# Kernel optimization log

Hardware: AMD Instinct MI355X
Metric: run time of the kernel (lower is better)

Reference implementation:

```python
import jax, jax.numpy as jnp
import numpy as np

DIM = 1024
D_STATE = 16
D_CONV = 4
EXPAND = 2
D_INNER = EXPAND * DIM          # 2048
DT_RANK = (DIM + 15) // 16      # 64 (math.ceil(d_model/16))
BSZ = 2
SEQ = 2048


def setup_inputs() -> dict:
    key = jax.random.key(0)
    ks = jax.random.split(key, 8)
    g = lambda k, shape, scale: (jax.random.normal(k, shape, jnp.float32) * scale)
    return {
        "x": g(ks[0], (BSZ, SEQ, DIM), 1.0),
        # in_proj: Linear(d_model -> 2*d_inner, bias=False)
        "W_in": g(ks[1], (2 * D_INNER, DIM), DIM ** -0.5),
        # depthwise causal conv1d: groups=d_inner, kernel d_conv, bias=True
        "conv_w": g(ks[2], (D_INNER, 1, D_CONV), D_CONV ** -0.5),
        "conv_b": jnp.zeros((D_INNER,), jnp.float32),
        # x_proj: Linear(d_inner -> dt_rank + 2*d_state, bias=False)
        "W_xproj": g(ks[3], (DT_RANK + 2 * D_STATE, D_INNER), D_INNER ** -0.5),
        # dt_proj: Linear(dt_rank -> d_inner, bias=True)
        "W_dt": g(ks[4], (D_INNER, DT_RANK), DT_RANK ** -0.5),
        "b_dt": g(ks[5], (D_INNER,), 0.1),
        # S4D-real init: A = -exp(A_log), A_log = log(1..d_state)
        "A_log": jnp.log(jnp.broadcast_to(
            jnp.arange(1, D_STATE + 1, dtype=jnp.float32), (D_INNER, D_STATE))),
        "D": jnp.ones((D_INNER,), jnp.float32),
        # out_proj: Linear(d_inner -> d_model, bias=False)
        "W_out": g(ks[6], (DIM, D_INNER), D_INNER ** -0.5),
        # wrapper LayerNorm(dim)
        "gamma": jnp.ones((DIM,), jnp.float32),
        "beta": jnp.zeros((DIM,), jnp.float32),
    }


def reference(x, W_in, conv_w, conv_b, W_xproj, W_dt, b_dt,
              A_log, D, W_out, gamma, beta):
    B, L, _ = x.shape
    # ---- input projection, split into conv path and gate ----
    xz = x @ W_in.T                              # (B, L, 2*d_inner)
    xc, z = jnp.split(xz, 2, axis=-1)
    # ---- depthwise causal conv1d + SiLU ----
    xt = jnp.transpose(xc, (0, 2, 1))            # (B, d_inner, L)
    conv = jax.lax.conv_general_dilated(
        xt, conv_w, window_strides=(1,), padding=[(D_CONV - 1, 0)],
        dimension_numbers=("NCH", "OIH", "NCH"), feature_group_count=D_INNER)
    u = jax.nn.silu(jnp.transpose(conv + conv_b[None, :, None], (0, 2, 1)))  # (B,L,d_inner)
    # ---- input-dependent delta, B, C ----
    xdbc = u @ W_xproj.T                          # (B, L, dt_rank + 2*d_state)
    dt = xdbc[..., :DT_RANK]
    Bm = xdbc[..., DT_RANK:DT_RANK + D_STATE]     # (B, L, d_state)
    Cm = xdbc[..., DT_RANK + D_STATE:]            # (B, L, d_state)
    delta = jax.nn.softplus(dt @ W_dt.T + b_dt)   # (B, L, d_inner)
    A = -jnp.exp(A_log)                           # (d_inner, d_state)
    # ---- selective scan: h_t = exp(dt*A) h_{t-1} + dt*B_t*u_t ; y_t = <h_t, C_t> ----
    def step(h, inputs):
        d_t, u_t, B_t, C_t = inputs               # (B,d_inner),(B,d_inner),(B,S),(B,S)
        dA = jnp.exp(d_t[:, :, None] * A)         # (B, d_inner, S)
        h = h * dA + (d_t * u_t)[:, :, None] * B_t[:, None, :]
        y = jnp.einsum("bds,bs->bd", h, C_t)
        return h, y
    tm = lambda a: jnp.transpose(a, (1, 0, 2))    # time-major for scan
    h0 = jnp.zeros((B, D_INNER, D_STATE), x.dtype)
    _, ys = jax.lax.scan(step, h0, (tm(delta), tm(u), tm(Bm), tm(Cm)))
    y = jnp.transpose(ys, (1, 0, 2)) + u * D      # skip term D*u
    y = y * jax.nn.silu(z)                        # gate
    out = y @ W_out.T                             # (B, L, dim)
    # ---- wrapper LayerNorm(dim), eps=1e-5 ----
    mean = out.mean(-1, keepdims=True)
    var = out.var(-1, keepdims=True)
    return (out - mean) * jax.lax.rsqrt(var + 1e-5) * gamma + beta
```

## Files before the change

### kernel.cpp

```cpp
#include <hip/hip_runtime.h>
#include <stdint.h>

typedef unsigned short u16;
typedef __bf16 bf16x8 __attribute__((ext_vector_type(8)));
typedef unsigned short u16x8 __attribute__((ext_vector_type(8)));
typedef unsigned short u16x4 __attribute__((ext_vector_type(4)));
typedef float f32x4 __attribute__((ext_vector_type(4)));

#define BSZ 2
#define SEQ 2048
#define DIM 1024
#define D_INNER 2048
#define DT_RANK 64
#define D_STATE 16
#define XPROJ_N 96
#define NCHUNK 32
#define CHUNK_T 64
#define LOG2E 1.44269504f

#define N_X   4194304
#define N_W   4194304
#define N_WX  196608
#define N_WDT 131072
#define N_WO  2097152
#define N_XD  393216

__device__ __forceinline__ float bf2f(u16 h) {
    return __uint_as_float(((unsigned)h) << 16);
}
__device__ __forceinline__ u16 f2bf(float f) {
    unsigned u = __float_as_uint(f);
    unsigned r = (u + 0x7FFFu + ((u >> 16) & 1u)) >> 16;
    return (u16)r;
}

__device__ __forceinline__ f32x4 mfma16(bf16x8 a, bf16x8 b, f32x4 c) {
    return __builtin_amdgcn_mfma_f32_16x16x32_bf16(a, b, c, 0, 0, 0);
}

__device__ __forceinline__ void gload_lds16(const void* g, void* l) {
    __builtin_amdgcn_global_load_lds(
        (const __attribute__((address_space(1))) unsigned int*)(uintptr_t)g,
        (__attribute__((address_space(3))) unsigned int*)(uintptr_t)l,
        16, 0, 0);
}

__device__ __forceinline__ void split4(const float* __restrict__ in,
                                       u16* __restrict__ hi, u16* __restrict__ lo,
                                       long i)
{
    f32x4 v = *(const f32x4*)(in + i);
    u16x4 h, l;
    #pragma unroll
    for (int j = 0; j < 4; j++) {
        u16 hh = f2bf(v[j]);
        h[j] = hh;
        l[j] = f2bf(v[j] - bf2f(hh));
    }
    *(u16x4*)(hi + i) = h;
    *(u16x4*)(lo + i) = l;
}

__global__ __launch_bounds__(256)
void megasplit4(const float* __restrict__ x,  u16* __restrict__ xh,  u16* __restrict__ xl,
                const float* __restrict__ w,  u16* __restrict__ wh,  u16* __restrict__ wl,
                const float* __restrict__ wx, u16* __restrict__ wxh, u16* __restrict__ wxl,
                const float* __restrict__ wd, u16* __restrict__ wdh, u16* __restrict__ wdl)
{
    long i = ((long)blockIdx.x * 256 + threadIdx.x) * 4;
    if (i < N_X) { split4(x, xh, xl, i); return; }
    i -= N_X;
    if (i < N_W) { split4(w, wh, wl, i); return; }
    i -= N_W;
    if (i < N_WX) { split4(wx, wxh, wxl, i); return; }
    i -= N_WX;
    if (i < N_WDT) { split4(wd, wdh, wdl, i); }
}

__global__ __launch_bounds__(512, 2)
void gemm256_xz(const u16* __restrict__ xh, const u16* __restrict__ xl,
                const u16* __restrict__ wh, const u16* __restrict__ wl,
                u16* __restrict__ xc, float* __restrict__ z)
{
    __shared__ u16 lds[49152];

    const int tid  = threadIdx.x;
    const int w    = tid >> 6;
    const int lane = tid & 63;
    const int r16  = lane & 15;
    const int quad = lane >> 4;
    const int wr   = w >> 2;
    const int wc   = w & 3;
    const long m0  = (long)blockIdx.y * 256;
    const long n0  = (long)blockIdx.x * 256;

    const int c0 = tid, c1 = tid + 512;
    const int ma0 = c0 >> 2, kc0 = ((c0 & 3) ^ ((ma0 >> 1) & 3)) * 8;
    const int ma1 = c1 >> 2, kc1 = ((c1 & 3) ^ ((ma1 >> 1) & 3)) * 8;
    const int arow0 = ((int)m0 + ma0) * DIM + kc0;
    const int arow1 = ((int)m0 + ma1) * DIM + kc1;
    const int brow0 = ((int)n0 + ma0) * DIM + kc0;
    const int brow1 = ((int)n0 + ma1) * DIM + kc1;

    int caof[8], cbof[4];
    #pragma unroll
    for (int i = 0; i < 8; i++) {
        int m = wr * 128 + i * 16 + r16;
        caof[i] = (m * 4 + (quad ^ ((m >> 1) & 3))) * 8;
    }
    #pragma unroll
    for (int j = 0; j < 4; j++) {
        int n = wc * 64 + j * 16 + r16;
        cbof[j] = (n * 4 + (quad ^ ((n >> 1) & 3))) * 8;
    }

    f32x4 acc[8][4];
    #pragma unroll
    for (int i = 0; i < 8; i++)
        #pragma unroll
        for (int j = 0; j < 4; j++) acc[i][j] = {0.f, 0.f, 0.f, 0.f};

    gload_lds16(xh + arow0,      lds + c0 * 8);
    gload_lds16(xh + arow1,      lds + c1 * 8);
    gload_lds16(wh + brow0,      lds + 24576 + c0 * 8);
    gload_lds16(wh + brow1,      lds + 24576 + c1 * 8);
    gload_lds16(xh + arow0 + 32, lds + 8192 + c0 * 8);
    gload_lds16(xh + arow1 + 32, lds + 8192 + c1 * 8);
    gload_lds16(wh + brow0 + 32, lds + 24576 + 8192 + c0 * 8);
    gload_lds16(wh + brow1 + 32, lds + 24576 + 8192 + c1 * 8);
    asm volatile("s_waitcnt vmcnt(4)" ::: "memory");
    __builtin_amdgcn_s_barrier();

    int kt = 0;
#define XZ_ITER(CUR, SL)                                                      \
  {                                                                           \
    int st = kt + 2; if (st > 95) st = 95;                                    \
    const int ts = st >> 5;                                                   \
    const int kb = (st & 31) * 32;                                            \
    const u16* As = (ts < 2) ? xh : xl;                                       \
    const u16* Bs = (ts == 1) ? wl : wh;                                      \
    const u16* Alds = lds + (CUR) * 8192;                                     \
    const u16* Blds = lds + 24576 + (CUR) * 8192;                             \
      \
    bf16x8 bfr[4], afr[4];                                                    \
    _Pragma("unroll") for (int j = 0; j < 4; j++)                             \
        bfr[j] = *(const bf16x8*)(Blds + cbof[j]);                            \
    _Pragma("unroll") for (int i = 0; i < 4; i++)                             \
        afr[i] = *(const bf16x8*)(Alds + caof[i]);                            \
    gload_lds16(As + arow0 + kb, lds + (SL) * 8192 + c0 * 8);                 \
    gload_lds16(As + arow1 + kb, lds + (SL) * 8192 + c1 * 8);                 \
    __builtin_amdgcn_sched_barrier(0);                                        \
    __builtin_amdgcn_s_barrier();                                             \
    asm volatile("s_waitcnt lgkmcnt(0)" ::: "memory");                        \
    __builtin_amdgcn_sched_barrier(0);                                        \
    __builtin_amdgcn_s_setprio(1);                                            \
    _Pragma("unroll") for (int i = 0; i < 4; i++)                             \
      _Pragma("unroll") for (int j = 0; j < 4; j++)                           \
        acc[i][j] = mfma16(afr[i], bfr[j], acc[i][j]);                        \
    __builtin_amdgcn_s_setprio(0);                                            \
    __builtin_amdgcn_sched_barrier(0);                                        \
    __builtin_amdgcn_s_barrier();                                             \
            \
    bf16x8 af2[4];                                                            \
    _Pragma("unroll") for (int i = 0; i < 4; i++)                             \
        af2[i] = *(const bf16x8*)(Alds + caof[4 + i]);                        \
    gload_lds16(Bs + brow0 + kb, lds + 24576 + (SL) * 8192 + c0 * 8);         \
    gload_lds16(Bs + brow1 + kb, lds + 24576 + (SL) * 8192 + c1 * 8);         \
    __builtin_amdgcn_sched_barrier(0);                                        \
    __builtin_amdgcn_s_barrier();                                             \
    asm volatile("s_waitcnt lgkmcnt(0)" ::: "memory");                        \
    __builtin_amdgcn_sched_barrier(0);                                        \
    __builtin_amdgcn_s_setprio(1);                                            \
    _Pragma("unroll") for (int i = 0; i < 4; i++)                             \
      _Pragma("unroll") for (int j = 0; j < 4; j++)                           \
        acc[4 + i][j] = mfma16(af2[i], bfr[j], acc[4 + i][j]);                \
    __builtin_amdgcn_s_setprio(0);                                            \
    __builtin_amdgcn_sched_barrier(0);                                        \
    asm volatile("s_waitcnt vmcnt(4)" ::: "memory");                          \
    __builtin_amdgcn_s_barrier();                                             \
    kt++;                                                                     \
  }

    #pragma unroll 1
    for (int it = 0; it < 32; it++) {
        XZ_ITER(0, 2)
        XZ_ITER(1, 0)
        XZ_ITER(2, 1)
    }
#undef XZ_ITER

    asm volatile("s_waitcnt vmcnt(0)" ::: "memory");

    const bool isz = (n0 >= 2048);
    #pragma unroll
    for (int i = 0; i < 8; i++) {
        #pragma unroll
        for (int j = 0; j < 4; j++) {
            long col = n0 + wc * 64 + j * 16 + r16;
            #pragma unroll
            for (int r = 0; r < 4; r++) {
                long row = m0 + wr * 128 + i * 16 + quad * 4 + r;
                if (!isz) xc[row * (long)D_INNER + col] = f2bf(acc[i][j][r]);
                else      z[row * (long)D_INNER + (col - D_INNER)] = acc[i][j][r];
            }
        }
    }
}

__global__ __launch_bounds__(512, 2)
void gemm256_out(const u16* __restrict__ A, const u16* __restrict__ Bh,
                 const u16* __restrict__ Bl, float* __restrict__ OutBase)
{
    __shared__ u16 lds[49152];

    const int tid  = threadIdx.x;
    const int w    = tid >> 6;
    const int lane = tid & 63;
    const int r16  = lane & 15;
    const int quad = lane >> 4;
    const int wr   = w >> 2;
    const int wc   = w & 3;
    const long m0  = (long)blockIdx.y * 256;
    const long n0  = (long)blockIdx.x * 256;
    const int  kz  = blockIdx.z;
    const u16* Bs  = (kz >= 2) ? Bl : Bh;
    const int  kbase = (kz & 1) * 1024;
    float* Out = OutBase + (long)kz * 4194304;

    const int c0 = tid, c1 = tid + 512;
    const int ma0 = c0 >> 2, kc0 = ((c0 & 3) ^ ((ma0 >> 1) & 3)) * 8;
    const int ma1 = c1 >> 2, kc1 = ((c1 & 3) ^ ((ma1 >> 1) & 3)) * 8;
    const int arow0 = ((int)m0 + ma0) * D_INNER + kbase + kc0;
    const int arow1 = ((int)m0 + ma1) * D_INNER + kbase + kc1;
    const int brow0 = ((int)n0 + ma0) * D_INNER + kbase + kc0;
    const int brow1 = ((int)n0 + ma1) * D_INNER + kbase + kc1;

    int caof[8], cbof[4];
    #pragma unroll
    for (int i = 0; i < 8; i++) {
        int m = wr * 128 + i * 16 + r16;
        caof[i] = (m * 4 + (quad ^ ((m >> 1) & 3))) * 8;
    }
    #pragma unroll
    for (int j = 0; j < 4; j++) {
        int n = wc * 64 + j * 16 + r16;
        cbof[j] = (n * 4 + (quad ^ ((n >> 1) & 3))) * 8;
    }

    f32x4 acc[8][4];
    #pragma unroll
    for (int i = 0; i < 8; i++)
        #pragma unroll
        for (int j = 0; j < 4; j++) acc[i][j] = {0.f, 0.f, 0.f, 0.f};

    gload_lds16(A  + arow0,      lds + c0 * 8);
    gload_lds16(A  + arow1,      lds + c1 * 8);
    gload_lds16(Bs + brow0,      lds + 24576 + c0 * 8);
    gload_lds16(Bs + brow1,      lds + 24576 + c1 * 8);
    gload_lds16(A  + arow0 + 32, lds + 8192 + c0 * 8);
    gload_lds16(A  + arow1 + 32, lds + 8192 + c1 * 8);
    gload_lds16(Bs + brow0 + 32, lds + 24576 + 8192 + c0 * 8);
    gload_lds16(Bs + brow1 + 32, lds + 24576 + 8192 + c1 * 8);
    asm volatile("s_waitcnt vmcnt(4)" ::: "memory");
    __builtin_amdgcn_s_barrier();

    int kt = 0;
#define OUT_ITER(CUR, SL)                                                     \
  {                                                                           \
    int st = kt + 2; if (st > 31) st = 31;                                    \
    const int kb = st * 32;                                                   \
    const u16* Alds = lds + (CUR) * 8192;                                     \
    const u16* Blds = lds + 24576 + (CUR) * 8192;                             \
    bf16x8 bfr[4], afr[4];                                                    \
    _Pragma("unroll") for (int j = 0; j < 4; j++)                             \
        bfr[j] = *(const bf16x8*)(Blds + cbof[j]);                            \
    _Pragma("unroll") for (int i = 0; i < 4; i++)                             \
        afr[i] = *(const bf16x8*)(Alds + caof[i]);                            \
    gload_lds16(A + arow0 + kb, lds + (SL) * 8192 + c0 * 8);                  \
    gload_lds16(A + arow1 + kb, lds + (SL) * 8192 + c1 * 8);                  \
    __builtin_amdgcn_sched_barrier(0);                                        \
    __builtin_amdgcn_s_barrier();                                             \
    asm volatile("s_waitcnt lgkmcnt(0)" ::: "memory");                        \
    __builtin_amdgcn_sched_barrier(0);                                        \
    __builtin_amdgcn_s_setprio(1);                                            \
    _Pragma("unroll") for (int i = 0; i < 4; i++)                             \
      _Pragma("unroll") for (int j = 0; j < 4; j++)                           \
        acc[i][j] = mfma16(afr[i], bfr[j], acc[i][j]);                        \
    __builtin_amdgcn_s_setprio(0);                                            \
    __builtin_amdgcn_sched_barrier(0);                                        \
    __builtin_amdgcn_s_barrier();                                             \
    bf16x8 af2[4];                                                            \
    _Pragma("unroll") for (int i = 0; i < 4; i++)                             \
        af2[i] = *(const bf16x8*)(Alds + caof[4 + i]);                        \
    gload_lds16(Bs + brow0 + kb, lds + 24576 + (SL) * 8192 + c0 * 8);         \
    gload_lds16(Bs + brow1 + kb, lds + 24576 + (SL) * 8192 + c1 * 8);         \
    __builtin_amdgcn_sched_barrier(0);                                        \
    __builtin_amdgcn_s_barrier();                                             \
    asm volatile("s_waitcnt lgkmcnt(0)" ::: "memory");                        \
    __builtin_amdgcn_sched_barrier(0);                                        \
    __builtin_amdgcn_s_setprio(1);                                            \
    _Pragma("unroll") for (int i = 0; i < 4; i++)                             \
      _Pragma("unroll") for (int j = 0; j < 4; j++)                           \
        acc[4 + i][j] = mfma16(af2[i], bfr[j], acc[4 + i][j]);                \
    __builtin_amdgcn_s_setprio(0);                                            \
    __builtin_amdgcn_sched_barrier(0);                                        \
    asm volatile("s_waitcnt vmcnt(4)" ::: "memory");                          \
    __builtin_amdgcn_s_barrier();                                             \
    kt++;                                                                     \
  }

    #pragma unroll 1
    for (int it = 0; it < 10; it++) {
        OUT_ITER(0, 2)
        OUT_ITER(1, 0)
        OUT_ITER(2, 1)
    }
    OUT_ITER(0, 2)
    OUT_ITER(1, 0)
#undef OUT_ITER

    asm volatile("s_waitcnt vmcnt(0)" ::: "memory");

    #pragma unroll
    for (int i = 0; i < 8; i++) {
        #pragma unroll
        for (int j = 0; j < 4; j++) {
            long col = n0 + wc * 64 + j * 16 + r16;
            #pragma unroll
            for (int r = 0; r < 4; r++) {
                long row = m0 + wr * 128 + i * 16 + quad * 4 + r;
                Out[row * (long)DIM + col] = acc[i][j][r];
            }
        }
    }
}

__global__ __launch_bounds__(64)
void gemm_dt32(const u16* __restrict__ Ah, const u16* __restrict__ Al, int lda,
               const u16* __restrict__ Bh, const u16* __restrict__ Bl, int ldb,
               float* __restrict__ C, int ldc, const float* __restrict__ bias)
{
    const int lane = threadIdx.x;
    const int r16  = lane & 15;
    const int quad = lane >> 4;
    const long m0 = (long)blockIdx.y * 32;
    const long n0 = (long)blockIdx.x * 32;

    const u16* Ah0 = Ah + (m0 + r16) * (long)lda + quad * 8;
    const u16* Ah1 = Ah0 + 16L * lda;
    const u16* Al0 = Al + (m0 + r16) * (long)lda + quad * 8;
    const u16* Al1 = Al0 + 16L * lda;
    const u16* Bh0 = Bh + (n0 + r16) * (long)ldb + quad * 8;
    const u16* Bh1 = Bh0 + 16L * ldb;
    const u16* Bl0 = Bl + (n0 + r16) * (long)ldb + quad * 8;
    const u16* Bl1 = Bl0 + 16L * ldb;

    f32x4 acc00 = {0,0,0,0}, acc01 = {0,0,0,0}, acc10 = {0,0,0,0}, acc11 = {0,0,0,0};

    #pragma unroll
    for (int k = 0; k < DT_RANK; k += 32) {
        bf16x8 a0h = *(const bf16x8*)(Ah0 + k);
        bf16x8 a1h = *(const bf16x8*)(Ah1 + k);
        bf16x8 a0l = *(const bf16x8*)(Al0 + k);
        bf16x8 a1l = *(const bf16x8*)(Al1 + k);
        bf16x8 b0h = *(const bf16x8*)(Bh0 + k);
        bf16x8 b1h = *(const bf16x8*)(Bh1 + k);
        bf16x8 b0l = *(const bf16x8*)(Bl0 + k);
        bf16x8 b1l = *(const bf16x8*)(Bl1 + k);
        acc00 = mfma16(a0h, b0h, acc00); acc00 = mfma16(a0h, b0l, acc00); acc00 = mfma16(a0l, b0h, acc00);
        acc01 = mfma16(a0h, b1h, acc01); acc01 = mfma16(a0h, b1l, acc01); acc01 = mfma16(a0l, b1h, acc01);
        acc10 = mfma16(a1h, b0h, acc10); acc10 = mfma16(a1h, b0l, acc10); acc10 = mfma16(a1l, b0h, acc10);
        acc11 = mfma16(a1h, b1h, acc11); acc11 = mfma16(a1h, b1l, acc11); acc11 = mfma16(a1l, b1h, acc11);
    }

    #pragma unroll
    for (int i = 0; i < 2; i++) {
        #pragma unroll
        for (int j = 0; j < 2; j++) {
            f32x4 v = (i == 0) ? (j == 0 ? acc00 : acc01) : (j == 0 ? acc10 : acc11);
            long col = n0 + j * 16 + r16;
            #pragma unroll
            for (int r = 0; r < 4; r++) {
                long row = m0 + i * 16 + quad * 4 + r;
                float x = v[r] + bias[col];
                x = (x > 15.f) ? x : log1pf(__expf(x));
                C[row * (long)ldc + col] = x;
            }
        }
    }
}

__global__ __launch_bounds__(64)
void gemm3_skp(const u16* __restrict__ A, int lda,
               const u16* __restrict__ Bh, const u16* __restrict__ Bl, int ldb,
               float* __restrict__ Cpart, int ldc, int K0)
{
    const int lane = threadIdx.x;
    const int r16  = lane & 15;
    const int quad = lane >> 4;
    const long m0 = (long)blockIdx.y * 32;
    const long n0 = (long)blockIdx.x * 32;
    const int kbase = blockIdx.z * K0;
    float* C = Cpart + (long)blockIdx.z * N_XD;

    const u16* Ap0 = A  + (m0 + r16) * (long)lda + quad * 8 + kbase;
    const u16* Ap1 = Ap0 + 16L * lda;
    const u16* Bh0 = Bh + (n0 + r16) * (long)ldb + quad * 8 + kbase;
    const u16* Bh1 = Bh0 + 16L * ldb;
    const u16* Bl0 = Bl + (n0 + r16) * (long)ldb + quad * 8 + kbase;
    const u16* Bl1 = Bl0 + 16L * ldb;

    f32x4 acc00 = {0,0,0,0}, acc01 = {0,0,0,0}, acc10 = {0,0,0,0}, acc11 = {0,0,0,0};

    for (int k = 0; k < K0; k += 32) {
        bf16x8 a0 = *(const bf16x8*)(Ap0 + k);
        bf16x8 a1 = *(const bf16x8*)(Ap1 + k);
        bf16x8 b0h = *(const bf16x8*)(Bh0 + k);
        bf16x8 b1h = *(const bf16x8*)(Bh1 + k);
        bf16x8 b0l = *(const bf16x8*)(Bl0 + k);
        bf16x8 b1l = *(const bf16x8*)(Bl1 + k);
        acc00 = mfma16(a0, b0h, acc00); acc00 = mfma16(a0, b0l, acc00);
        acc01 = mfma16(a0, b1h, acc01); acc01 = mfma16(a0, b1l, acc01);
        acc10 = mfma16(a1, b0h, acc10); acc10 = mfma16(a1, b0l, acc10);
        acc11 = mfma16(a1, b1h, acc11); acc11 = mfma16(a1, b1l, acc11);
    }

    #pragma unroll
    for (int i = 0; i < 2; i++) {
        #pragma unroll
        for (int j = 0; j < 2; j++) {
            f32x4 v = (i == 0) ? (j == 0 ? acc00 : acc01) : (j == 0 ? acc10 : acc11);
            long col = n0 + j * 16 + r16;
            #pragma unroll
            for (int r = 0; r < 4; r++) {
                long row = m0 + i * 16 + quad * 4 + r;
                C[row * (long)ldc + col] = v[r];
            }
        }
    }
}

__global__ __launch_bounds__(256)
void combine3(const float* __restrict__ part, float* __restrict__ xdbc,
              u16* __restrict__ hi, u16* __restrict__ lo)
{
    long i = ((long)blockIdx.x * 256 + threadIdx.x) * 4;
    if (i >= N_XD) return;
    f32x4 s = *(const f32x4*)(part + i);
    #pragma unroll
    for (int j = 1; j < 8; j++) {
        f32x4 p = *(const f32x4*)(part + (long)j * N_XD + i);
        s[0] += p[0]; s[1] += p[1]; s[2] += p[2]; s[3] += p[3];
    }
    *(f32x4*)(xdbc + i) = s;
    u16x4 h, l;
    #pragma unroll
    for (int j = 0; j < 4; j++) {
        u16 hh = f2bf(s[j]);
        h[j] = hh;
        l[j] = f2bf(s[j] - bf2f(hh));
    }
    *(u16x4*)(hi + i) = h;
    *(u16x4*)(lo + i) = l;
}

__global__ __launch_bounds__(256)
void conv_silu(const u16* __restrict__ xc, const float* __restrict__ cw,
               const float* __restrict__ cb, u16* __restrict__ u)
{
    long idx = ((long)blockIdx.x * 256 + threadIdx.x) * 8;
    int t  = (int)((idx >> 11) & 2047);
    int d0 = (int)(idx & 2047);

    bf16x8 xrow[4];
    #pragma unroll
    for (int j = 0; j < 4; j++) {
        int tt = t - 3 + j;
        if (tt >= 0) xrow[j] = *(const bf16x8*)(xc + idx + (long)(j - 3) * D_INNER);
        else         xrow[j] = bf16x8{0,0,0,0,0,0,0,0};
    }
    u16x8 out;
    #pragma unroll
    for (int e = 0; e < 8; e++) {
        int d = d0 + e;
        float acc = cb[d];
        #pragma unroll
        for (int j = 0; j < 4; j++)
            acc += cw[d * 4 + j] * (float)xrow[j][e];
        out[e] = f2bf(acc / (1.f + __expf(-acc)));
    }
    *(u16x8*)(u + idx) = out;
}

__global__ __launch_bounds__(256)
void scan_partA(const float* __restrict__ delta, const u16* __restrict__ u,
                const float* __restrict__ xdbc, const float* __restrict__ A_log,
                float* __restrict__ hbuf, float* __restrict__ sdelta,
                const float* __restrict__ wout, u16* __restrict__ wouth,
                u16* __restrict__ woutl)
{
    const int d = blockIdx.x * 256 + threadIdx.x;
    const int c = blockIdx.y;
    const int b = blockIdx.z;
    const int t0 = c * CHUNK_T;

    float Af[16];
    #pragma unroll
    for (int s = 0; s < 16; s++) Af[s] = -__expf(A_log[d * 16 + s]) * LOG2E;

    float h[16];
    #pragma unroll
    for (int s = 0; s < 16; s++) h[s] = 0.f;
    float sd = 0.f;

    const float* dptr = delta + ((long)b * SEQ + t0) * D_INNER + d;
    const u16*   uptr = u     + ((long)b * SEQ + t0) * D_INNER + d;
    const float* xp   = xdbc  + ((long)b * SEQ + t0) * XPROJ_N;

    for (int t = 0; t < CHUNK_T; t++) {
        float dl = dptr[(long)t * D_INNER];
        float uu = bf2f(uptr[(long)t * D_INNER]);
        f32x4 B0 = *(const f32x4*)(xp + t * XPROJ_N + DT_RANK);
        f32x4 B1 = *(const f32x4*)(xp + t * XPROJ_N + DT_RANK + 4);
        f32x4 B2 = *(const f32x4*)(xp + t * XPROJ_N + DT_RANK + 8);
        f32x4 B3 = *(const f32x4*)(xp + t * XPROJ_N + DT_RANK + 12);
        float Bv[16] = {B0[0],B0[1],B0[2],B0[3], B1[0],B1[1],B1[2],B1[3],
                        B2[0],B2[1],B2[2],B2[3], B3[0],B3[1],B3[2],B3[3]};
        sd += dl;
        float dlu = dl * uu;
        #pragma unroll
        for (int s = 0; s < 16; s++)
            h[s] = h[s] * exp2f(dl * Af[s]) + dlu * Bv[s];
    }

    float* hout = hbuf + ((long)(b * NCHUNK + c) * D_INNER + d) * 16;
    #pragma unroll
    for (int s = 0; s < 16; s++) hout[s] = h[s];
    sdelta[(long)(b * NCHUNK + c) * D_INNER + d] = sd;

    long tidg = (((long)b * NCHUNK + c) * 8 + blockIdx.x) * 256 + threadIdx.x;
    long base = tidg * 16;
    #pragma unroll
    for (int k = 0; k < 4; k++) split4(wout, wouth, woutl, base + 4 * k);
}

__global__ __launch_bounds__(256)
void scan_fixup(float* __restrict__ hbuf, const float* __restrict__ sdelta,
                const float* __restrict__ A_log)
{
    const int idx = blockIdx.x * 256 + threadIdx.x;
    const int ds = idx & (D_INNER * 16 - 1);
    const int b  = idx >> 15;
    const float Af = -__expf(A_log[ds]) * LOG2E;
    float hin = 0.f;
    #pragma unroll 4
    for (int c = 0; c < NCHUNK; c++) {
        long gi = (long)(b * NCHUNK + c) * (D_INNER * 16) + ds;
        float e = hbuf[gi];
        hbuf[gi] = hin;
        float sd = sdelta[(long)(b * NCHUNK + c) * D_INNER + (ds >> 4)];
        hin = e + exp2f(Af * sd) * hin;
    }
}

__global__ __launch_bounds__(256)
void scan_partC(const float* __restrict__ delta, const u16* __restrict__ u,
                const float* __restrict__ xdbc, const float* __restrict__ z,
                const float* __restrict__ A_log, const float* __restrict__ Dp,
                const float* __restrict__ hbuf, u16* __restrict__ y)
{
    const int d = blockIdx.x * 256 + threadIdx.x;
    const int c = blockIdx.y;
    const int b = blockIdx.z;
    const int t0 = c * CHUNK_T;

    float Af[16];
    #pragma unroll
    for (int s = 0; s < 16; s++) Af[s] = -__expf(A_log[d * 16 + s]) * LOG2E;
    const float Dd = Dp[d];

    float h[16];
    const float* hin = hbuf + ((long)(b * NCHUNK + c) * D_INNER + d) * 16;
    #pragma unroll
    for (int s = 0; s < 16; s++) h[s] = hin[s];

    const float* dptr = delta + ((long)b * SEQ + t0) * D_INNER + d;
    const u16*   uptr = u     + ((long)b * SEQ + t0) * D_INNER + d;
    const float* zptr = z     + ((long)b * SEQ + t0) * D_INNER + d;
    const float* xp   = xdbc  + ((long)b * SEQ + t0) * XPROJ_N;
    u16* yptr = y + ((long)b * SEQ + t0) * D_INNER + d;

    for (int t = 0; t < CHUNK_T; t++) {
        float dl = dptr[(long)t * D_INNER];
        float uu = bf2f(uptr[(long)t * D_INNER]);
        float zl = zptr[(long)t * D_INNER];
        f32x4 B0 = *(const f32x4*)(xp + t * XPROJ_N + DT_RANK);
        f32x4 B1 = *(const f32x4*)(xp + t * XPROJ_N + DT_RANK + 4);
        f32x4 B2 = *(const f32x4*)(xp + t * XPROJ_N + DT_RANK + 8);
        f32x4 B3 = *(const f32x4*)(xp + t * XPROJ_N + DT_RANK + 12);
        f32x4 C0 = *(const f32x4*)(xp + t * XPROJ_N + DT_RANK + 16);
        f32x4 C1 = *(const f32x4*)(xp + t * XPROJ_N + DT_RANK + 20);
        f32x4 C2 = *(const f32x4*)(xp + t * XPROJ_N + DT_RANK + 24);
        f32x4 C3 = *(const f32x4*)(xp + t * XPROJ_N + DT_RANK + 28);
        float Bv[16] = {B0[0],B0[1],B0[2],B0[3], B1[0],B1[1],B1[2],B1[3],
                        B2[0],B2[1],B2[2],B2[3], B3[0],B3[1],B3[2],B3[3]};
        float Cv[16] = {C0[0],C0[1],C0[2],C0[3], C1[0],C1[1],C1[2],C1[3],
                        C2[0],C2[1],C2[2],C2[3], C3[0],C3[1],C3[2],C3[3]};
        float dlu = dl * uu;
        float p0 = 0.f, p1 = 0.f, p2 = 0.f, p3 = 0.f;
        #pragma unroll
        for (int s = 0; s < 16; s += 4) {
            h[s]   = h[s]   * exp2f(dl * Af[s])   + dlu * Bv[s];
            h[s+1] = h[s+1] * exp2f(dl * Af[s+1]) + dlu * Bv[s+1];
            h[s+2] = h[s+2] * exp2f(dl * Af[s+2]) + dlu * Bv[s+2];
            h[s+3] = h[s+3] * exp2f(dl * Af[s+3]) + dlu * Bv[s+3];
            p0 += h[s]   * Cv[s];
            p1 += h[s+1] * Cv[s+1];
            p2 += h[s+2] * Cv[s+2];
            p3 += h[s+3] * Cv[s+3];
        }
        float acc = (p0 + p1) + (p2 + p3);
        float sz = zl / (1.f + __expf(-zl));
        float yy = (acc + uu * Dd) * sz;
        yptr[(long)t * D_INNER] = f2bf(yy);
    }
}

__global__ __launch_bounds__(256)
void layernorm_kernel(const float* __restrict__ p0,
                      const float* __restrict__ gamma, const float* __restrict__ beta,
                      float* __restrict__ out)
{
    const long row = blockIdx.x;
    const long base = row * DIM;
    int tid = threadIdx.x;
    float v[4];
    float sum = 0.f, sq = 0.f;
    #pragma unroll
    for (int i = 0; i < 4; i++) {
        long c = base + tid + i * 256;
        v[i] = (p0[c] + p0[c + 4194304]) + (p0[c + 8388608] + p0[c + 12582912]);
        sum += v[i];
        sq  += v[i] * v[i];
    }
    #pragma unroll
    for (int off = 1; off < 64; off <<= 1) {
        sum += __shfl_xor(sum, off);
        sq  += __shfl_xor(sq, off);
    }
    __shared__ float ssum[4], ssq[4];
    int w = tid >> 6;
    if ((tid & 63) == 0) { ssum[w] = sum; ssq[w] = sq; }
    __syncthreads();
    float ts = ssum[0] + ssum[1] + ssum[2] + ssum[3];
    float tq = ssq[0] + ssq[1] + ssq[2] + ssq[3];
    float mean = ts * (1.f / DIM);
    float var  = tq * (1.f / DIM) - mean * mean;
    float rstd = rsqrtf(var + 1e-5f);
    float* o = out + base;
    #pragma unroll
    for (int i = 0; i < 4; i++) {
        int c = tid + i * 256;
        o[c] = (v[i] - mean) * rstd * gamma[c] + beta[c];
    }
}

extern "C" void kernel_launch(void* const* d_in, const int* in_sizes, int n_in,
                              void* d_out, int out_size, void* d_ws, size_t ws_size,
                              hipStream_t stream)
{
    const float* x      = (const float*)d_in[0];
    const float* W_in   = (const float*)d_in[1];
    const float* conv_w = (const float*)d_in[2];
    const float* conv_b = (const float*)d_in[3];
    const float* W_xproj= (const float*)d_in[4];
    const float* W_dt   = (const float*)d_in[5];
    const float* b_dt   = (const float*)d_in[6];
    const float* A_log  = (const float*)d_in[7];
    const float* Dv     = (const float*)d_in[8];
    const float* W_out  = (const float*)d_in[9];
    const float* gamma  = (const float*)d_in[10];
    const float* beta   = (const float*)d_in[11];

    char* ws = (char*)d_ws;
    u16*   xc    = (u16*)(ws);
    float* g3p   = (float*)(ws);
    u16*   xdh   = (u16*)(ws + 12582912);
    u16*   xdl   = (u16*)(ws + 14155776);
    float* hbuf  = (float*)(ws);
    u16*   wouth = (u16*)(ws + 8388608);
    u16*   woutl = (u16*)(ws + 12582912);
    float* z     = (float*)(ws + 16777216);
    float* opre  = (float*)(ws + 16777216);
    u16*   u     = (u16*)(ws + 50331648);
    u16*   xh    = (u16*)(ws + 67108864);
    u16*   xl    = (u16*)(ws + 75497472);
    u16*   wh    = (u16*)(ws + 83886080);
    u16*   wl    = (u16*)(ws + 92274688);
    float* delta = (float*)(ws + 67108864);
    float* xdbc  = (float*)(ws + 100663296);
    u16*   wxh   = (u16*)(ws + 102236160);
    u16*   wxl   = (u16*)(ws + 102629376);
    u16*   wdth  = (u16*)(ws + 103022592);
    u16*   wdtl  = (u16*)(ws + 103284736);
    float* sdel  = (float*)(ws + 103546880);
    u16*   yb    = (u16*)d_out;

    megasplit4<<<8512, 256, 0, stream>>>(x, xh, xl, W_in, wh, wl,
                                         W_xproj, wxh, wxl, W_dt, wdth, wdtl);
    gemm256_xz<<<dim3(16, 16), 512, 0, stream>>>(xh, xl, wh, wl, xc, z);
    conv_silu<<<4096, 256, 0, stream>>>(xc, conv_w, conv_b, u);
    gemm3_skp<<<dim3(3, 128, 8), 64, 0, stream>>>(
        u, D_INNER, wxh, wxl, D_INNER, g3p, XPROJ_N, 256);
    combine3<<<384, 256, 0, stream>>>(g3p, xdbc, xdh, xdl);
    gemm_dt32<<<dim3(64, 128), 64, 0, stream>>>(
        xdh, xdl, XPROJ_N, wdth, wdtl, DT_RANK, delta, D_INNER, b_dt);
    scan_partA<<<dim3(8, NCHUNK, BSZ), 256, 0, stream>>>(
        delta, u, xdbc, A_log, hbuf, sdel, W_out, wouth, woutl);
    scan_fixup<<<256, 256, 0, stream>>>(hbuf, sdel, A_log);
    scan_partC<<<dim3(8, NCHUNK, BSZ), 256, 0, stream>>>(delta, u, xdbc, z, A_log, Dv, hbuf, yb);
    gemm256_out<<<dim3(4, 16, 4), 512, 0, stream>>>(yb, wouth, woutl, opre);
    layernorm_kernel<<<4096, 256, 0, stream>>>(opre, gamma, beta, (float*)d_out);
}
```

Baseline: 440.2 us.

## Reuse hi/lo LDS tiles across split-bf16 product terms in xz GEMM

Result: faster. 429.6 us (-2.4%).

```diff
diff --git a/kernel.cpp b/kernel.cpp
--- a/kernel.cpp
+++ b/kernel.cpp
@@ -77,12 +77,23 @@
     if (i < N_WDT) { split4(wd, wdh, wdl, i); }
 }
 
+#define PH_TOP                                                                \
+    __builtin_amdgcn_sched_barrier(0);                                        \
+    __builtin_amdgcn_s_barrier();                                             \
+    asm volatile("s_waitcnt lgkmcnt(0)" ::: "memory");                        \
+    __builtin_amdgcn_sched_barrier(0);                                        \
+    __builtin_amdgcn_s_setprio(1);
+#define PH_BOT                                                                \
+    __builtin_amdgcn_s_setprio(0);                                            \
+    __builtin_amdgcn_sched_barrier(0);                                        \
+    __builtin_amdgcn_s_barrier();
+
 __global__ __launch_bounds__(512, 2)
 void gemm256_xz(const u16* __restrict__ xh, const u16* __restrict__ xl,
                 const u16* __restrict__ wh, const u16* __restrict__ wl,
                 u16* __restrict__ xc, float* __restrict__ z)
 {
-    __shared__ u16 lds[49152];
+    __shared__ u16 lds[65536];
 
     const int tid  = threadIdx.x;
     const int w    = tid >> 6;
@@ -120,74 +131,98 @@
         #pragma unroll
         for (int j = 0; j < 4; j++) acc[i][j] = {0.f, 0.f, 0.f, 0.f};
 
-    gload_lds16(xh + arow0,      lds + c0 * 8);
-    gload_lds16(xh + arow1,      lds + c1 * 8);
-    gload_lds16(wh + brow0,      lds + 24576 + c0 * 8);
-    gload_lds16(wh + brow1,      lds + 24576 + c1 * 8);
-    gload_lds16(xh + arow0 + 32, lds + 8192 + c0 * 8);
-    gload_lds16(xh + arow1 + 32, lds + 8192 + c1 * 8);
-    gload_lds16(wh + brow0 + 32, lds + 24576 + 8192 + c0 * 8);
-    gload_lds16(wh + brow1 + 32, lds + 24576 + 8192 + c1 * 8);
-    asm volatile("s_waitcnt vmcnt(4)" ::: "memory");
+    gload_lds16(xh + arow0, lds + c0 * 8);
+    gload_lds16(xh + arow1, lds + c1 * 8);
+    gload_lds16(xl + arow0, lds + 8192 + c0 * 8);
+    gload_lds16(xl + arow1, lds + 8192 + c1 * 8);
+    gload_lds16(wh + brow0, lds + 16384 + c0 * 8);
+    gload_lds16(wh + brow1, lds + 16384 + c1 * 8);
+    gload_lds16(wl + brow0, lds + 24576 + c0 * 8);
+    gload_lds16(wl + brow1, lds + 24576 + c1 * 8);
+    asm volatile("s_waitcnt vmcnt(0)" ::: "memory");
     __builtin_amdgcn_s_barrier();
 
     int kt = 0;
-#define XZ_ITER(CUR, SL)                                                      \
+#define XZ_FTILE(CUR, SN)                                                     \
   {                                                                           \
-    int st = kt + 2; if (st > 95) st = 95;                                    \
-    const int ts = st >> 5;                                                   \
-    const int kb = (st & 31) * 32;                                            \
-    const u16* As = (ts < 2) ? xh : xl;                                       \
-    const u16* Bs = (ts == 1) ? wl : wh;                                      \
-    const u16* Alds = lds + (CUR) * 8192;                                     \
-    const u16* Blds = lds + 24576 + (CUR) * 8192;                             \
-      \
-    bf16x8 bfr[4], afr[4];                                                    \
+    int st = kt + 1; if (st > 31) st = 31;                                    \
+    const int kb = st * 32;                                                   \
+    const u16* AHp = lds + (CUR) * 32768;                                     \
+    const u16* ALp = AHp + 8192;                                              \
+    const u16* BHp = AHp + 16384;                                             \
+    const u16* BLp = AHp + 24576;                                             \
+    u16* Sb = lds + (SN) * 32768;                                             \
+    bf16x8 a0[4], a1[4], fb[4];                                               \
+                            \
     _Pragma("unroll") for (int j = 0; j < 4; j++)                             \
-        bfr[j] = *(const bf16x8*)(Blds + cbof[j]);                            \
-    _Pragma("unroll") for (int i = 0; i < 4; i++)                             \
-        afr[i] = *(const bf16x8*)(Alds + caof[i]);                            \
-    gload_lds16(As + arow0 + kb, lds + (SL) * 8192 + c0 * 8);                 \
-    gload_lds16(As + arow1 + kb, lds + (SL) * 8192 + c1 * 8);                 \
-    __builtin_amdgcn_sched_barrier(0);                                        \
-    __builtin_amdgcn_s_barrier();                                             \
-    asm volatile("s_waitcnt lgkmcnt(0)" ::: "memory");                        \
-    __builtin_amdgcn_sched_barrier(0);                                        \
-    __builtin_amdgcn_s_setprio(1);                                            \
+        fb[j] = *(const bf16x8*)(BHp + cbof[j]);                              \
+    _Pragma("unroll") for (int i = 0; i < 4; i++)                             \
+        a0[i] = *(const bf16x8*)(AHp + caof[i]);                              \
+    gload_lds16(xh + arow0 + kb, Sb + c0 * 8);                                \
+    gload_lds16(xh + arow1 + kb, Sb + c1 * 8);                                \
+    PH_TOP                                                                    \
     _Pragma("unroll") for (int i = 0; i < 4; i++)                             \
       _Pragma("unroll") for (int j = 0; j < 4; j++)                           \
-        acc[i][j] = mfma16(afr[i], bfr[j], acc[i][j]);                        \
+        acc[i][j] = mfma16(a0[i], fb[j], acc[i][j]);                          \
+    PH_BOT                                                                    \
+                                \
+    _Pragma("unroll") for (int i = 0; i < 4; i++)                             \
+        a1[i] = *(const bf16x8*)(AHp + caof[4 + i]);                          \
+    gload_lds16(xl + arow0 + kb, Sb + 8192 + c0 * 8);                         \
+    gload_lds16(xl + arow1 + kb, Sb + 8192 + c1 * 8);                         \
+    PH_TOP                                                                    \
+    _Pragma("unroll") for (int i = 0; i < 4; i++)                             \
+      _Pragma("unroll") for (int j = 0; j < 4; j++)                           \
+        acc[4 + i][j] = mfma16(a1[i], fb[j], acc[4 + i][j]);                  \
+    PH_BOT                                                                    \
+                        \
+    _Pragma("unroll") for (int j = 0; j < 4; j++)                             \
+        fb[j] = *(const bf16x8*)(BLp + cbof[j]);                              \
+    gload_lds16(wh + brow0 + kb, Sb + 16384 + c0 * 8);                        \
+    gload_lds16(wh + brow1 + kb, Sb + 16384 + c1 * 8);                        \
+    PH_TOP                                                                    \
+    _Pragma("unroll") for (int i = 0; i < 4; i++)                             \
+      _Pragma("unroll") for (int j = 0; j < 4; j++)                           \
+        acc[i][j] = mfma16(a0[i], fb[j], acc[i][j]);                          \
+    PH_BOT                                                                    \
+                             \
+    gload_lds16(wl + brow0 + kb, Sb + 24576 + c0 * 8);                        \
+    gload_lds16(wl + brow1 + kb, Sb + 24576 + c1 * 8);                        \
+    PH_TOP                                                                    \
+    _Pragma("unroll") for (int i = 0; i < 4; i++)                             \
+      _Pragma("unroll") for (int j = 0; j < 4; j++)                           \
+        acc[4 + i][j] = mfma16(a1[i], fb[j], acc[4 + i][j]);                  \
+    PH_BOT                                                                    \
+                              \
+    _Pragma("unroll") for (int j = 0; j < 4; j++)                             \
+        fb[j] = *(const bf16x8*)(BHp + cbof[j]);                              \
+    _Pragma("unroll") for (int i = 0; i < 4; i++)                             \
+        a0[i] = *(const bf16x8*)(ALp + caof[i]);                              \
+    PH_TOP                                                                    \
+    _Pragma("unroll") for (int i = 0; i < 4; i++)                             \
+      _Pragma("unroll") for (int j = 0; j < 4; j++)                           \
+        acc[i][j] = mfma16(a0[i], fb[j], acc[i][j]);                          \
+    PH_BOT                                                                    \
+                 \
+    _Pragma("unroll") for (int i = 0; i < 4; i++)                             \
+        a1[i] = *(const bf16x8*)(ALp + caof[4 + i]);                          \
+    PH_TOP                                                                    \
+    _Pragma("unroll") for (int i = 0; i < 4; i++)                             \
+      _Pragma("unroll") for (int j = 0; j < 4; j++)                           \
+        acc[4 + i][j] = mfma16(a1[i], fb[j], acc[4 + i][j]);                  \
     __builtin_amdgcn_s_setprio(0);                                            \
     __builtin_amdgcn_sched_barrier(0);                                        \
-    __builtin_amdgcn_s_barrier();                                             \
-            \
-    bf16x8 af2[4];                                                            \
-    _Pragma("unroll") for (int i = 0; i < 4; i++)                             \
-        af2[i] = *(const bf16x8*)(Alds + caof[4 + i]);                        \
-    gload_lds16(Bs + brow0 + kb, lds + 24576 + (SL) * 8192 + c0 * 8);         \
-    gload_lds16(Bs + brow1 + kb, lds + 24576 + (SL) * 8192 + c1 * 8);         \
-    __builtin_amdgcn_sched_barrier(0);                                        \
-    __builtin_amdgcn_s_barrier();                                             \
-    asm volatile("s_waitcnt lgkmcnt(0)" ::: "memory");                        \
-    __builtin_amdgcn_sched_barrier(0);                                        \
-    __builtin_amdgcn_s_setprio(1);                                            \
-    _Pragma("unroll") for (int i = 0; i < 4; i++)                             \
-      _Pragma("unroll") for (int j = 0; j < 4; j++)                           \
-        acc[4 + i][j] = mfma16(af2[i], bfr[j], acc[4 + i][j]);                \
-    __builtin_amdgcn_s_setprio(0);                                            \
-    __builtin_amdgcn_sched_barrier(0);                                        \
-    asm volatile("s_waitcnt vmcnt(4)" ::: "memory");                          \
+    asm volatile("s_waitcnt vmcnt(0)" ::: "memory");                          \
     __builtin_amdgcn_s_barrier();                                             \
     kt++;                                                                     \
   }
 
     #pragma unroll 1
-    for (int it = 0; it < 32; it++) {
-        XZ_ITER(0, 2)
-        XZ_ITER(1, 0)
-        XZ_ITER(2, 1)
-    }
-#undef XZ_ITER
+    for (int it = 0; it < 16; it++) {
+        XZ_FTILE(0, 1)
+        XZ_FTILE(1, 0)
+    }
+#undef XZ_FTILE
 
     asm volatile("s_waitcnt vmcnt(0)" ::: "memory");
 
@@ -278,27 +313,17 @@
         afr[i] = *(const bf16x8*)(Alds + caof[i]);                            \
     gload_lds16(A + arow0 + kb, lds + (SL) * 8192 + c0 * 8);                  \
     gload_lds16(A + arow1 + kb, lds + (SL) * 8192 + c1 * 8);                  \
-    __builtin_amdgcn_sched_barrier(0);                                        \
-    __builtin_amdgcn_s_barrier();                                             \
-    asm volatile("s_waitcnt lgkmcnt(0)" ::: "memory");                        \
-    __builtin_amdgcn_sched_barrier(0);                                        \
-    __builtin_amdgcn_s_setprio(1);                                            \
+    PH_TOP                                                                    \
     _Pragma("unroll") for (int i = 0; i < 4; i++)                             \
       _Pragma("unroll") for (int j = 0; j < 4; j++)                           \
         acc[i][j] = mfma16(afr[i], bfr[j], acc[i][j]);                        \
-    __builtin_amdgcn_s_setprio(0);                                            \
-    __builtin_amdgcn_sched_barrier(0);                                        \
-    __builtin_amdgcn_s_barrier();                                             \
+    PH_BOT                                                                    \
     bf16x8 af2[4];                                                            \
     _Pragma("unroll") for (int i = 0; i < 4; i++)                             \
         af2[i] = *(const bf16x8*)(Alds + caof[4 + i]);                        \
     gload_lds16(Bs + brow0 + kb, lds + 24576 + (SL) * 8192 + c0 * 8);         \
     gload_lds16(Bs + brow1 + kb, lds + 24576 + (SL) * 8192 + c1 * 8);         \
-    __builtin_amdgcn_sched_barrier(0);                                        \
-    __builtin_amdgcn_s_barrier();                                             \
-    asm volatile("s_waitcnt lgkmcnt(0)" ::: "memory");                        \
-    __builtin_amdgcn_sched_barrier(0);                                        \
-    __builtin_amdgcn_s_setprio(1);                                            \
+    PH_TOP                                                                    \
     _Pragma("unroll") for (int i = 0; i < 4; i++)                             \
       _Pragma("unroll") for (int j = 0; j < 4; j++)                           \
         acc[4 + i][j] = mfma16(af2[i], bfr[j], acc[4 + i][j]);                \
```
